# Optimization experiments

Hardware: AMD Instinct MI355X
Metric: run time of the kernel (lower is better)

The kernel has to match this reference:

```python
import jax, jax.numpy as jnp
import numpy as np

# Output shape from ToDenseMink.__init__:
#   batch=4, out_size=256, x = 512 // (2//1) = 256, y = 512 // (2//1) = 256
B, C, X, Y = 4, 256, 256, 256
N = 200000  # number of occupied sparse cells


def setup_inputs() -> dict:
    key = jax.random.key(0)
    kf, kc = jax.random.split(key)
    feats = jax.random.normal(kf, (N, C), dtype=jnp.float32)
    # Unique (batch, x, y) coordinates so the scatter is well-defined
    # (MinkowskiEngine sparse tensors have unique coordinates).
    lin = jax.random.permutation(kc, B * X * Y)[:N]
    b = lin // (X * Y)
    rem = lin % (X * Y)
    x = rem // Y
    y = rem % Y
    coords = jnp.stack([b, x, y], axis=-1).astype(jnp.int32)  # [N, 3]
    return {"feats": feats, "coords": coords}


def reference(feats, coords):
    # Equivalent of x.dense(shape=[B, C, X, Y], min_coordinate=0)[0]:
    # scatter each feature row into the dense grid at (batch, :, x, y).
    dense = jnp.zeros((B, C, X, Y), dtype=feats.dtype)
    dense = dense.at[coords[:, 0], :, coords[:, 1], coords[:, 2]].set(
        feats, mode="drop"
    )
    return dense
```

## Files before the change

kernel.cpp:

```cpp
#include <hip/hip_runtime.h>

#define BB 4
#define CC 256
#define XX 256
#define YY 256
#define NCELLS (BB * XX * YY)

#define CH 32
#define NCHUNK (CC / CH)

__global__ void k_fill_idx(int4* __restrict__ idx4) {
    int i = blockIdx.x * blockDim.x + threadIdx.x;
    idx4[i] = make_int4(-1, -1, -1, -1);
}

__global__ void k_scatter_idx(const int* __restrict__ coords,
                              int* __restrict__ idx, int n) {
    int i = blockIdx.x * blockDim.x + threadIdx.x;
    if (i >= n) return;
    int b = coords[i * 3 + 0];
    int x = coords[i * 3 + 1];
    int y = coords[i * 3 + 2];
    if ((unsigned)b < BB && (unsigned)x < XX && (unsigned)y < YY) {
        idx[(b * XX + x) * YY + y] = i;
    }
}

__global__ __launch_bounds__(256, 4) void k_gather_out(
        const float4* __restrict__ feats4,
        const int*    __restrict__ idx,
        float*        __restrict__ out) {
    __shared__ int   rowid[YY];
    __shared__ float lds[CH][YY];

    const int bx = blockIdx.x;
    const int t  = threadIdx.x;
    const int b  = bx >> 8;
    const int x  = bx & 255;

    rowid[t] = idx[bx * YY + t];
    __syncthreads();

    const int lane = t & 63;
    const int w    = t >> 6;
    const int sub  = lane & 7;
    const int g    = lane >> 3;

    const size_t out_base = ((size_t)b * CC * XX + x) * YY;

    for (int ch = 0; ch < NCHUNK; ++ch) {
        const int c0 = ch * CH;

        #pragma unroll
        for (int j = 0; j < 8; ++j) {
            const int y = w * 64 + j * 8 + g;
            const int r = rowid[y];
            const bool valid = (r >= 0);
            float4 v = feats4[(size_t)(valid ? r : 0) * (CC / 4)
                              + (c0 >> 2) + sub];
            if (!valid) { v.x = 0.f; v.y = 0.f; v.z = 0.f; v.w = 0.f; }
            const int cl = sub * 4;
            const int ys = y ^ (cl & 28);
            lds[cl + 0][ys] = v.x;
            lds[cl + 1][ys] = v.y;
            lds[cl + 2][ys] = v.z;
            lds[cl + 3][ys] = v.w;
        }
        __syncthreads();

        #pragma unroll
        for (int k = 0; k < 8; ++k) {
            const int cl = w * 8 + k;
            const int c  = c0 + cl;
            const int ys = (lane * 4) ^ (cl & 28);
            const float4 v = *(const float4*)&lds[cl][ys];
            *(float4*)&out[out_base + (size_t)c * (XX * YY) + lane * 4] = v;
        }
        __syncthreads();
    }
}

extern "C" void kernel_launch(void* const* d_in, const int* in_sizes, int n_in,
                              void* d_out, int out_size, void* d_ws, size_t ws_size,
                              hipStream_t stream) {
    const float* feats  = (const float*)d_in[0];
    const int*   coords = (const int*)d_in[1];
    int n = in_sizes[1] / 3;

    int*   idx = (int*)d_ws;
    float* out = (float*)d_out;

    k_fill_idx<<<NCELLS / 4 / 256, 256, 0, stream>>>((int4*)idx);

    k_scatter_idx<<<(n + 255) / 256, 256, 0, stream>>>(coords, idx, n);

    k_gather_out<<<BB * XX, 256, 0, stream>>>((const float4*)feats, idx, out);
}
```

Measured before the change: 414.3 us.

## Tile gather kernel over y-chunks with full-row feature loads

Changes the gather kernel's chunking from 32 channels across all y to 32 y positions across all 256 channels. Each wave now loads a whole contiguous feature row per y, with all loads issued before the LDS writes, and transposes through a swizzled LDS tile. Output stores become 128-byte segments per channel instead of full 1 KB rows, and LDS reads become scalar. This trades better read coalescing for smaller write segments and more LDS instructions.

```diff
diff --git a/kernel.cpp b/kernel.cpp
--- a/kernel.cpp
+++ b/kernel.cpp
@@ -6,8 +6,8 @@
 #define YY 256
 #define NCELLS (BB * XX * YY)
 
-#define CH 32
-#define NCHUNK (CC / CH)
+#define YCH 32
+#define NYCH (YY / YCH)
 
 __global__ void k_fill_idx(int4* __restrict__ idx4) {
     int i = blockIdx.x * blockDim.x + threadIdx.x;
@@ -31,7 +31,7 @@
         const int*    __restrict__ idx,
         float*        __restrict__ out) {
     __shared__ int   rowid[YY];
-    __shared__ float lds[CH][YY];
+    __shared__ float lds[YCH][CC];
 
     const int bx = blockIdx.x;
     const int t  = threadIdx.x;
@@ -43,38 +43,43 @@
 
     const int lane = t & 63;
     const int w    = t >> 6;
-    const int sub  = lane & 7;
     const int g    = lane >> 3;
+    const int m    = lane & 7;
 
     const size_t out_base = ((size_t)b * CC * XX + x) * YY;
 
-    for (int ch = 0; ch < NCHUNK; ++ch) {
-        const int c0 = ch * CH;
+    for (int yc = 0; yc < NYCH; ++yc) {
+        const int y0 = yc * YCH;
 
+        float4 v[8];
         #pragma unroll
         for (int j = 0; j < 8; ++j) {
-            const int y = w * 64 + j * 8 + g;
-            const int r = rowid[y];
+            const int yl = w * 8 + j;
+            const int r  = rowid[y0 + yl];
             const bool valid = (r >= 0);
-            float4 v = feats4[(size_t)(valid ? r : 0) * (CC / 4)
-                              + (c0 >> 2) + sub];
-            if (!valid) { v.x = 0.f; v.y = 0.f; v.z = 0.f; v.w = 0.f; }
-            const int cl = sub * 4;
-            const int ys = y ^ (cl & 28);
-            lds[cl + 0][ys] = v.x;
-            lds[cl + 1][ys] = v.y;
-            lds[cl + 2][ys] = v.z;
-            lds[cl + 3][ys] = v.w;
+            v[j] = feats4[(size_t)(valid ? r : 0) * (CC / 4) + lane];
+            if (!valid) { v[j].x = 0.f; v[j].y = 0.f; v[j].z = 0.f; v[j].w = 0.f; }
+        }
+        #pragma unroll
+        for (int j = 0; j < 8; ++j) {
+            const int yl = w * 8 + j;
+            const int S  = ((yl >> 1) & 7) << 2;
+            *(float4*)&lds[yl][(4 * lane) ^ S] = v[j];
         }
         __syncthreads();
 
         #pragma unroll
         for (int k = 0; k < 8; ++k) {
-            const int cl = w * 8 + k;
-            const int c  = c0 + cl;
-            const int ys = (lane * 4) ^ (cl & 28);
-            const float4 v = *(const float4*)&lds[cl][ys];
-            *(float4*)&out[out_base + (size_t)c * (XX * YY) + lane * 4] = v;
+            const int c = k * 32 + w * 8 + g;
+            float4 o;
+            {
+                const int y0l = 4 * m;
+                o.x = lds[y0l + 0][c ^ ((((y0l + 0) >> 1) & 7) << 2)];
+                o.y = lds[y0l + 1][c ^ ((((y0l + 1) >> 1) & 7) << 2)];
+                o.z = lds[y0l + 2][c ^ ((((y0l + 2) >> 1) & 7) << 2)];
+                o.w = lds[y0l + 3][c ^ ((((y0l + 3) >> 1) & 7) << 2)];
+            }
+            *(float4*)&out[out_base + (size_t)c * (XX * YY) + y0 + 4 * m] = o;
         }
         __syncthreads();
     }
```

Measured after the change: 418.9 us. Within noise of the previous version (+1.1%).
